# Kernel tuning notes

Measured on AMD Instinct MI355X. Metric: run time of the kernel, lower is better.

Reference implementation:

```python
import jax, jax.numpy as jnp
import numpy as np

B, N, L, S, H, E = 4, 8, 512, 512, 8, 64  # e == d (value head dim)


def setup_inputs() -> dict:
    key = jax.random.key(0)
    ks = jax.random.split(key, 6)
    shp_q = (B, N, L, H, E)
    shp_kv = (B, N, S, H, E)
    return {
        "q_re": jax.random.normal(ks[0], shp_q, dtype=jnp.float32),
        "q_im": jax.random.normal(ks[1], shp_q, dtype=jnp.float32),
        "k_re": jax.random.normal(ks[2], shp_kv, dtype=jnp.float32),
        "k_im": jax.random.normal(ks[3], shp_kv, dtype=jnp.float32),
        "v_re": jax.random.normal(ks[4], shp_kv, dtype=jnp.float32),
        "v_im": jax.random.normal(ks[5], shp_kv, dtype=jnp.float32),
    }


def reference(q_re, q_im, k_re, k_im, v_re, v_im):
    # complex_mul('bnlhe,bnshe->bnhls', q, k):
    #   real = qr.kr - qi.ki ; imag = qr.ki - qi.kr  (note: NOT standard +; faithful to source)
    s_re = (jnp.einsum('bnlhe,bnshe->bnhls', q_re, k_re)
            - jnp.einsum('bnlhe,bnshe->bnhls', q_im, k_im))
    s_im = (jnp.einsum('bnlhe,bnshe->bnhls', q_re, k_im)
            - jnp.einsum('bnlhe,bnshe->bnhls', q_im, k_re))
    # softmax over |scores| along key axis s (no 1/sqrt(e) scaling in source)
    mag = jnp.sqrt(s_re * s_re + s_im * s_im)
    attn = jax.nn.softmax(mag, axis=-1)  # [b,n,h,l,s]; dropout = identity (eval)
    # scores are real-valued after softmax; complex_mul with zero imag reduces to:
    v_out_re = jnp.einsum('bnhls,bnshd->bnlhd', attn, v_re)
    v_out_im = jnp.einsum('bnhls,bnshd->bnlhd', attn, v_im)
    # stack real/imag (torch returns complex tensor) -> [2,b,n,l,h,d]
    return jnp.stack((v_out_re, v_out_im), axis=0)
```

## Files before the change

kernel.cpp:

```cpp
#include <hip/hip_runtime.h>
#include <hip/hip_fp16.h>

typedef _Float16 half8 __attribute__((ext_vector_type(8)));
typedef _Float16 half4 __attribute__((ext_vector_type(4)));
typedef __fp16  fp16x2 __attribute__((ext_vector_type(2)));
typedef float f32x4 __attribute__((ext_vector_type(4)));

#define BB 4
#define NB 8
#define LL 512
#define SS 512
#define HH 8
#define EE 64
#define ROWSTRIDE (HH * EE)

__device__ __forceinline__ unsigned pkh(float a, float b) {
    union { fp16x2 h; unsigned u; } c;
    c.h = __builtin_amdgcn_cvt_pkrtz(a, b);
    return c.u;
}


__global__ __launch_bounds__(512, 4) void cattn_kernel(
    const float* __restrict__ qre, const float* __restrict__ qim,
    const float* __restrict__ kre, const float* __restrict__ kim,
    const float* __restrict__ vre, const float* __restrict__ vim,
    float* __restrict__ out)
{
    __shared__ __align__(16) _Float16 KtRe[2][64 * 64];
    __shared__ __align__(16) _Float16 KtIm[2][64 * 64];
    __shared__ __align__(16) _Float16 VtRe[2][64 * 64];
    __shared__ __align__(16) _Float16 VtIm[2][64 * 64];
    __shared__ __align__(16) _Float16 Pbuf[8][16 * 64];

    const int tid  = threadIdx.x;
    const int wave = tid >> 6;
    const int lane = tid & 63;
    const int lgrp = lane >> 4;
    const int l16  = lane & 15;

    const int bid  = blockIdx.x;
    const int nid  = (bid & 7) * 128 + (bid >> 3);
    const int lt   = nid & 3;
    const int head = nid >> 2;
    const int h    = head & 7;
    const int bn   = head >> 3;

    const size_t headQ = (size_t)bn * LL * ROWSTRIDE + (size_t)h * EE;
    const size_t headK = (size_t)bn * SS * ROWSTRIDE + (size_t)h * EE;

    float4 ka[2], kb[2];
    float4 vv[4];

    const int kEc0  = tid & 7;
    const int kS0   = (tid >> 3) & 63;
    const int vArr  = tid >> 8;
    const int vD0   = (tid & 15) * 4;
    const int vS0   = ((tid >> 4) & 15) * 4;

    auto stage_load = [&](int st) {
        const int tb = st * 64;
        {
            const float* p = kre + headK + (size_t)(tb + kS0) * ROWSTRIDE + kEc0 * 8;
            ka[0] = *(const float4*)p;
            kb[0] = *(const float4*)(p + 4);
        }
        {
            const float* p = kim + headK + (size_t)(tb + kS0) * ROWSTRIDE + kEc0 * 8;
            ka[1] = *(const float4*)p;
            kb[1] = *(const float4*)(p + 4);
        }
        {
            const float* src = vArr ? vim : vre;
            #pragma unroll
            for (int i = 0; i < 4; ++i)
                vv[i] = *(const float4*)(src + headK + (size_t)(tb + vS0 + i) * ROWSTRIDE + vD0);
        }
    };

    auto stage_write = [&](int buf) {
        #pragma unroll
        for (int it = 0; it < 2; ++it) {
            union { half8 h; unsigned u[4]; } kv;
            kv.u[0] = pkh(ka[it].x, ka[it].y);
            kv.u[1] = pkh(ka[it].z, ka[it].w);
            kv.u[2] = pkh(kb[it].x, kb[it].y);
            kv.u[3] = pkh(kb[it].z, kb[it].w);
            _Float16* base = it ? KtIm[buf] : KtRe[buf];
            *reinterpret_cast<half8*>(reinterpret_cast<char*>(base) +
                kS0 * 128 + ((kEc0 * 16) ^ ((kS0 & 7) << 4))) = kv.h;
        }
        {
            _Float16* base = vArr ? VtIm[buf] : VtRe[buf];
            #pragma unroll
            for (int dd = 0; dd < 4; ++dd) {
                int d = vD0 + dd;
                union { half4 h; unsigned u[2]; } hv;
                hv.u[0] = pkh((&vv[0].x)[dd], (&vv[1].x)[dd]);
                hv.u[1] = pkh((&vv[2].x)[dd], (&vv[3].x)[dd]);
                *reinterpret_cast<half4*>(reinterpret_cast<char*>(base) +
                    d * 128 + ((vS0 * 2) ^ ((d & 7) << 4))) = hv.h;
            }
        }
    };

    const int l0 = lt * 128 + wave * 16;
    half8 qr[2], qin[2];
    {
        size_t base = headQ + (size_t)(l0 + l16) * ROWSTRIDE + lgrp * 8;
        #pragma unroll
        for (int ec = 0; ec < 2; ++ec) {
            float4 a0 = *(const float4*)(qre + base + ec * 32);
            float4 a1 = *(const float4*)(qre + base + ec * 32 + 4);
            float4 b0 = *(const float4*)(qim + base + ec * 32);
            float4 b1 = *(const float4*)(qim + base + ec * 32 + 4);
            #pragma unroll
            for (int j = 0; j < 4; ++j) {
                qr[ec][j]      = (_Float16)((&a0.x)[j]);
                qr[ec][4 + j]  = (_Float16)((&a1.x)[j]);
                qin[ec][j]     = (_Float16)(-(&b0.x)[j]);
                qin[ec][4 + j] = (_Float16)(-(&b1.x)[j]);
            }
        }
    }

    f32x4 ore[4], oim[4];
    #pragma unroll
    for (int n = 0; n < 4; ++n) { ore[n] = (f32x4){0.f,0.f,0.f,0.f}; oim[n] = (f32x4){0.f,0.f,0.f,0.f}; }
    float m = -1e30f, lsum = 0.f;

    stage_load(0);
    stage_write(0);
    __syncthreads();

    char* Pw = reinterpret_cast<char*>(&Pbuf[wave][0]);
    const int prow = l16 * 128;
    const int pswz = (l16 & 7) << 4;

    for (int st = 0; st < 8; ++st) {
        const int cur = st & 1;
        if (st < 7) stage_load(st + 1);

        const char* KR = (const char*)KtRe[cur];
        const char* KI = (const char*)KtIm[cur];
        const char* VR = (const char*)VtRe[cur];
        const char* VI = (const char*)VtIm[cur];

        float p_[4][4];
        float tmax = 0.f;
        #pragma unroll
        for (int n = 0; n < 4; ++n) {
            int srow = n * 16 + l16;
            int rb   = srow * 128;
            int swz  = (srow & 7) << 4;
            half8 kr0 = *(const half8*)(KR + rb + ((lgrp * 16)      ^ swz));
            half8 kr1 = *(const half8*)(KR + rb + ((64 + lgrp * 16) ^ swz));
            half8 ki0 = *(const half8*)(KI + rb + ((lgrp * 16)      ^ swz));
            half8 ki1 = *(const half8*)(KI + rb + ((64 + lgrp * 16) ^ swz));
            f32x4 z = (f32x4){0.f,0.f,0.f,0.f};
            z = __builtin_amdgcn_mfma_f32_16x16x32_f16(kr0, qr[0],  z, 0, 0, 0);
            z = __builtin_amdgcn_mfma_f32_16x16x32_f16(kr1, qr[1],  z, 0, 0, 0);
            z = __builtin_amdgcn_mfma_f32_16x16x32_f16(ki0, qin[0], z, 0, 0, 0);
            z = __builtin_amdgcn_mfma_f32_16x16x32_f16(ki1, qin[1], z, 0, 0, 0);
            f32x4 w = (f32x4){0.f,0.f,0.f,0.f};
            w = __builtin_amdgcn_mfma_f32_16x16x32_f16(ki0, qr[0],  w, 0, 0, 0);
            w = __builtin_amdgcn_mfma_f32_16x16x32_f16(ki1, qr[1],  w, 0, 0, 0);
            w = __builtin_amdgcn_mfma_f32_16x16x32_f16(kr0, qin[0], w, 0, 0, 0);
            w = __builtin_amdgcn_mfma_f32_16x16x32_f16(kr1, qin[1], w, 0, 0, 0);
            #pragma unroll
            for (int r = 0; r < 4; ++r) {
                float mg = __builtin_amdgcn_sqrtf(z[r] * z[r] + w[r] * w[r]);
                p_[n][r] = mg;
                tmax = fmaxf(tmax, mg);
            }
        }

        tmax = fmaxf(tmax, __shfl_xor(tmax, 16));
        tmax = fmaxf(tmax, __shfl_xor(tmax, 32));
        float mn = fmaxf(m, tmax);
        if (__any(tmax > m)) {
            float sc = __expf(m - mn);
            lsum *= sc;
            float scr[4];
            #pragma unroll
            for (int r = 0; r < 4; ++r) scr[r] = __shfl(sc, lgrp * 4 + r);
            #pragma unroll
            for (int n = 0; n < 4; ++n)
                #pragma unroll
                for (int r = 0; r < 4; ++r) { ore[n][r] *= scr[r]; oim[n][r] *= scr[r]; }
        }
        m = mn;
        #pragma unroll
        for (int n = 0; n < 4; ++n)
            #pragma unroll
            for (int r = 0; r < 4; ++r) {
                float pe = __expf(p_[n][r] - mn);
                p_[n][r] = pe;
                lsum += pe;
            }

        #pragma unroll
        for (int n = 0; n < 4; ++n) {
            uint2 val;
            val.x = pkh(p_[n][0], p_[n][1]);
            val.y = pkh(p_[n][2], p_[n][3]);
            *reinterpret_cast<uint2*>(Pw + prow + ((n * 32 + lgrp * 8) ^ pswz)) = val;
        }

        #pragma unroll
        for (int kc = 0; kc < 2; ++kc) {
            half8 pa = *reinterpret_cast<const half8*>(Pw + prow + ((kc * 64 + lgrp * 16) ^ pswz));
            int sb2 = (kc * 32 + lgrp * 8) * 2;
            #pragma unroll
            for (int nd = 0; nd < 4; ++nd) {
                int d  = nd * 16 + l16;
                int vo = d * 128 + (sb2 ^ ((d & 7) << 4));
                half8 vr = *(const half8*)(VR + vo);
                half8 vi = *(const half8*)(VI + vo);
                ore[nd] = __builtin_amdgcn_mfma_f32_16x16x32_f16(pa, vr, ore[nd], 0, 0, 0);
                oim[nd] = __builtin_amdgcn_mfma_f32_16x16x32_f16(pa, vi, oim[nd], 0, 0, 0);
            }
        }

        if (st < 7) stage_write(cur ^ 1);
        __syncthreads();
    }

    lsum += __shfl_xor(lsum, 16);
    lsum += __shfl_xor(lsum, 32);
    const size_t outImOff = (size_t)BB * NB * LL * HH * EE;
    #pragma unroll
    for (int r = 0; r < 4; ++r) {
        int lrow = l0 + lgrp * 4 + r;
        float ls  = __shfl(lsum, lgrp * 4 + r);
        float inv = 1.f / ls;
        size_t obase = ((size_t)bn * LL + lrow) * ROWSTRIDE + (size_t)h * EE;
        #pragma unroll
        for (int nd = 0; nd < 4; ++nd) {
            int d = nd * 16 + l16;
            out[obase + d]            = ore[nd][r] * inv;
            out[outImOff + obase + d] = oim[nd][r] * inv;
        }
    }
}

extern "C" void kernel_launch(void* const* d_in, const int* in_sizes, int n_in,
                              void* d_out, int out_size, void* d_ws, size_t ws_size,
                              hipStream_t stream) {
    const float* qre = (const float*)d_in[0];
    const float* qim = (const float*)d_in[1];
    const float* kre = (const float*)d_in[2];
    const float* kim = (const float*)d_in[3];
    const float* vre = (const float*)d_in[4];
    const float* vim = (const float*)d_in[5];
    float* out = (float*)d_out;
    dim3 grid(1024), block(512);
    hipLaunchKernelGGL(cattn_kernel, grid, block, 0, stream,
                       qre, qim, kre, kim, vre, vim, out);
}
```

Baseline: 87.45 us.

## Software-pipeline QK scores of next tile with softmax/PV of current tile

Restructures the key-tile loop so the QK score MFMAs for tile t+1 are issued before the softmax and PV MFMAs for tile t, using two register sets of scores. This aims to overlap the exp/sqrt/shuffle work with matrix-core work and hide LDS latency. It adds an extra __syncthreads per stage and more live registers, which may cut occupancy under the 512x4 launch bound. The row-sum reduction now happens per tile.

```diff
diff --git a/kernel.cpp b/kernel.cpp
--- a/kernel.cpp
+++ b/kernel.cpp
@@ -20,6 +20,94 @@
     return c.u;
 }
 
+
+#define QK_PHASE(KRB, KIB, PP, MX) do {                                        \
+    float tmax_ = 0.f;                                                         \
+    const char* KR_ = (const char*)(KRB);                                      \
+    const char* KI_ = (const char*)(KIB);                                      \
+    _Pragma("unroll")                                                          \
+    for (int n = 0; n < 4; ++n) {                                              \
+        int srow = n * 16 + l16;                                               \
+        int rb   = srow * 128;                                                 \
+        int swz  = (srow & 7) << 4;                                            \
+        half8 kr0 = *(const half8*)(KR_ + rb + ((lgrp * 16)      ^ swz));      \
+        half8 kr1 = *(const half8*)(KR_ + rb + ((64 + lgrp * 16) ^ swz));      \
+        half8 ki0 = *(const half8*)(KI_ + rb + ((lgrp * 16)      ^ swz));      \
+        half8 ki1 = *(const half8*)(KI_ + rb + ((64 + lgrp * 16) ^ swz));      \
+        f32x4 z = (f32x4){0.f,0.f,0.f,0.f};                                    \
+        z = __builtin_amdgcn_mfma_f32_16x16x32_f16(kr0, qr[0],  z, 0, 0, 0);   \
+        z = __builtin_amdgcn_mfma_f32_16x16x32_f16(kr1, qr[1],  z, 0, 0, 0);   \
+        z = __builtin_amdgcn_mfma_f32_16x16x32_f16(ki0, qin[0], z, 0, 0, 0);   \
+        z = __builtin_amdgcn_mfma_f32_16x16x32_f16(ki1, qin[1], z, 0, 0, 0);   \
+        f32x4 w = (f32x4){0.f,0.f,0.f,0.f};                                    \
+        w = __builtin_amdgcn_mfma_f32_16x16x32_f16(ki0, qr[0],  w, 0, 0, 0);   \
+        w = __builtin_amdgcn_mfma_f32_16x16x32_f16(ki1, qr[1],  w, 0, 0, 0);   \
+        w = __builtin_amdgcn_mfma_f32_16x16x32_f16(kr0, qin[0], w, 0, 0, 0);   \
+        w = __builtin_amdgcn_mfma_f32_16x16x32_f16(kr1, qin[1], w, 0, 0, 0);   \
+        _Pragma("unroll")                                                      \
+        for (int r = 0; r < 4; ++r) {                                          \
+            float mg = __builtin_amdgcn_sqrtf(z[r] * z[r] + w[r] * w[r]);      \
+            PP[n][r] = mg;                                                     \
+            tmax_ = fmaxf(tmax_, mg);                                          \
+        }                                                                      \
+    }                                                                          \
+    MX = tmax_;                                                                \
+} while (0)
+
+#define FINISH_PHASE(VRB, VIB, PP, MX) do {                                    \
+    float tmax_ = fmaxf(MX, __shfl_xor(MX, 16));                               \
+    tmax_ = fmaxf(tmax_, __shfl_xor(tmax_, 32));                               \
+    float mn_ = fmaxf(m, tmax_);                                               \
+    if (__any(tmax_ > m)) {                                                    \
+        float sc_ = __expf(m - mn_);                                           \
+        lsum *= sc_;                                                           \
+        float scr_[4];                                                         \
+        _Pragma("unroll")                                                      \
+        for (int r = 0; r < 4; ++r) scr_[r] = __shfl(sc_, lgrp * 4 + r);       \
+        _Pragma("unroll")                                                      \
+        for (int n = 0; n < 4; ++n) {                                          \
+            _Pragma("unroll")                                                  \
+            for (int r = 0; r < 4; ++r) {                                      \
+                ore[n][r] *= scr_[r];                                          \
+                oim[n][r] *= scr_[r];                                          \
+            }                                                                  \
+        }                                                                      \
+    }                                                                          \
+    m = mn_;                                                                   \
+    float ps_ = 0.f;                                                           \
+    _Pragma("unroll")                                                          \
+    for (int n = 0; n < 4; ++n) {                                              \
+        _Pragma("unroll")                                                      \
+        for (int r = 0; r < 4; ++r) {                                          \
+            float pe_ = __expf(PP[n][r] - mn_);                                \
+            PP[n][r] = pe_;                                                    \
+            ps_ += pe_;                                                        \
+        }                                                                      \
+        uint2 val_;                                                            \
+        val_.x = pkh(PP[n][0], PP[n][1]);                                      \
+        val_.y = pkh(PP[n][2], PP[n][3]);                                      \
+        *reinterpret_cast<uint2*>(Pw + prow + ((n * 32 + lgrp * 8) ^ pswz)) = val_; \
+    }                                                                          \
+    ps_ += __shfl_xor(ps_, 16);                                                \
+    ps_ += __shfl_xor(ps_, 32);                                                \
+    lsum += ps_;                                                               \
+    const char* VR_ = (const char*)(VRB);                                      \
+    const char* VI_ = (const char*)(VIB);                                      \
+    _Pragma("unroll")                                                          \
+    for (int kc = 0; kc < 2; ++kc) {                                           \
+        half8 pa_ = *reinterpret_cast<const half8*>(Pw + prow + ((kc * 64 + lgrp * 16) ^ pswz)); \
+        int sb2_ = (kc * 32 + lgrp * 8) * 2;                                   \
+        _Pragma("unroll")                                                      \
+        for (int nd = 0; nd < 4; ++nd) {                                       \
+            int d_  = nd * 16 + l16;                                           \
+            int vo_ = d_ * 128 + (sb2_ ^ ((d_ & 7) << 4));                     \
+            half8 vr_ = *(const half8*)(VR_ + vo_);                            \
+            half8 vi_ = *(const half8*)(VI_ + vo_);                            \
+            ore[nd] = __builtin_amdgcn_mfma_f32_16x16x32_f16(pa_, vr_, ore[nd], 0, 0, 0); \
+            oim[nd] = __builtin_amdgcn_mfma_f32_16x16x32_f16(pa_, vi_, oim[nd], 0, 0, 0); \
+        }                                                                      \
+    }                                                                          \
+} while (0)
 
 __global__ __launch_bounds__(512, 4) void cattn_kernel(
     const float* __restrict__ qre, const float* __restrict__ qim,
@@ -129,105 +217,41 @@
     for (int n = 0; n < 4; ++n) { ore[n] = (f32x4){0.f,0.f,0.f,0.f}; oim[n] = (f32x4){0.f,0.f,0.f,0.f}; }
     float m = -1e30f, lsum = 0.f;
 
+    char* Pw = reinterpret_cast<char*>(&Pbuf[wave][0]);
+    const int prow = l16 * 128;
+    const int pswz = (l16 & 7) << 4;
+
+    float pA[4][4], pB[4][4];
+    float mxA, mxB;
+
     stage_load(0);
     stage_write(0);
     __syncthreads();
 
-    char* Pw = reinterpret_cast<char*>(&Pbuf[wave][0]);
-    const int prow = l16 * 128;
-    const int pswz = (l16 & 7) << 4;
-
-    for (int st = 0; st < 8; ++st) {
-        const int cur = st & 1;
-        if (st < 7) stage_load(st + 1);
-
-        const char* KR = (const char*)KtRe[cur];
-        const char* KI = (const char*)KtIm[cur];
-        const char* VR = (const char*)VtRe[cur];
-        const char* VI = (const char*)VtIm[cur];
-
-        float p_[4][4];
-        float tmax = 0.f;
-        #pragma unroll
-        for (int n = 0; n < 4; ++n) {
-            int srow = n * 16 + l16;
-            int rb   = srow * 128;
-            int swz  = (srow & 7) << 4;
-            half8 kr0 = *(const half8*)(KR + rb + ((lgrp * 16)      ^ swz));
-            half8 kr1 = *(const half8*)(KR + rb + ((64 + lgrp * 16) ^ swz));
-            half8 ki0 = *(const half8*)(KI + rb + ((lgrp * 16)      ^ swz));
-            half8 ki1 = *(const half8*)(KI + rb + ((64 + lgrp * 16) ^ swz));
-            f32x4 z = (f32x4){0.f,0.f,0.f,0.f};
-            z = __builtin_amdgcn_mfma_f32_16x16x32_f16(kr0, qr[0],  z, 0, 0, 0);
-            z = __builtin_amdgcn_mfma_f32_16x16x32_f16(kr1, qr[1],  z, 0, 0, 0);
-            z = __builtin_amdgcn_mfma_f32_16x16x32_f16(ki0, qin[0], z, 0, 0, 0);
-            z = __builtin_amdgcn_mfma_f32_16x16x32_f16(ki1, qin[1], z, 0, 0, 0);
-            f32x4 w = (f32x4){0.f,0.f,0.f,0.f};
-            w = __builtin_amdgcn_mfma_f32_16x16x32_f16(ki0, qr[0],  w, 0, 0, 0);
-            w = __builtin_amdgcn_mfma_f32_16x16x32_f16(ki1, qr[1],  w, 0, 0, 0);
-            w = __builtin_amdgcn_mfma_f32_16x16x32_f16(kr0, qin[0], w, 0, 0, 0);
-            w = __builtin_amdgcn_mfma_f32_16x16x32_f16(kr1, qin[1], w, 0, 0, 0);
-            #pragma unroll
-            for (int r = 0; r < 4; ++r) {
-                float mg = __builtin_amdgcn_sqrtf(z[r] * z[r] + w[r] * w[r]);
-                p_[n][r] = mg;
-                tmax = fmaxf(tmax, mg);
-            }
-        }
-
-        tmax = fmaxf(tmax, __shfl_xor(tmax, 16));
-        tmax = fmaxf(tmax, __shfl_xor(tmax, 32));
-        float mn = fmaxf(m, tmax);
-        if (__any(tmax > m)) {
-            float sc = __expf(m - mn);
-            lsum *= sc;
-            float scr[4];
-            #pragma unroll
-            for (int r = 0; r < 4; ++r) scr[r] = __shfl(sc, lgrp * 4 + r);
-            #pragma unroll
-            for (int n = 0; n < 4; ++n)
-                #pragma unroll
-                for (int r = 0; r < 4; ++r) { ore[n][r] *= scr[r]; oim[n][r] *= scr[r]; }
-        }
-        m = mn;
-        #pragma unroll
-        for (int n = 0; n < 4; ++n)
-            #pragma unroll
-            for (int r = 0; r < 4; ++r) {
-                float pe = __expf(p_[n][r] - mn);
-                p_[n][r] = pe;
-                lsum += pe;
-            }
-
-        #pragma unroll
-        for (int n = 0; n < 4; ++n) {
-            uint2 val;
-            val.x = pkh(p_[n][0], p_[n][1]);
-            val.y = pkh(p_[n][2], p_[n][3]);
-            *reinterpret_cast<uint2*>(Pw + prow + ((n * 32 + lgrp * 8) ^ pswz)) = val;
-        }
-
-        #pragma unroll
-        for (int kc = 0; kc < 2; ++kc) {
-            half8 pa = *reinterpret_cast<const half8*>(Pw + prow + ((kc * 64 + lgrp * 16) ^ pswz));
-            int sb2 = (kc * 32 + lgrp * 8) * 2;
-            #pragma unroll
-            for (int nd = 0; nd < 4; ++nd) {
-                int d  = nd * 16 + l16;
-                int vo = d * 128 + (sb2 ^ ((d & 7) << 4));
-                half8 vr = *(const half8*)(VR + vo);
-                half8 vi = *(const half8*)(VI + vo);
-                ore[nd] = __builtin_amdgcn_mfma_f32_16x16x32_f16(pa, vr, ore[nd], 0, 0, 0);
-                oim[nd] = __builtin_amdgcn_mfma_f32_16x16x32_f16(pa, vi, oim[nd], 0, 0, 0);
-            }
-        }
-
-        if (st < 7) stage_write(cur ^ 1);
+    stage_load(1);
+    QK_PHASE(KtRe[0], KtIm[0], pA, mxA);
+    stage_write(1);
+    __syncthreads();
+
+    for (int tp = 0; tp < 3; ++tp) {
+        stage_load(2 * tp + 2);
+        QK_PHASE(KtRe[1], KtIm[1], pB, mxB);
+        FINISH_PHASE(VtRe[0], VtIm[0], pA, mxA);
+        __syncthreads();
+        stage_write(0);
+        __syncthreads();
+        stage_load(2 * tp + 3);
+        QK_PHASE(KtRe[0], KtIm[0], pA, mxA);
+        FINISH_PHASE(VtRe[1], VtIm[1], pB, mxB);
+        __syncthreads();
+        stage_write(1);
         __syncthreads();
     }
 
-    lsum += __shfl_xor(lsum, 16);
-    lsum += __shfl_xor(lsum, 32);
+    QK_PHASE(KtRe[1], KtIm[1], pB, mxB);
+    FINISH_PHASE(VtRe[0], VtIm[0], pA, mxA);
+    FINISH_PHASE(VtRe[1], VtIm[1], pB, mxB);
+
     const size_t outImOff = (size_t)BB * NB * LL * HH * EE;
     #pragma unroll
     for (int r = 0; r < 4; ++r) {
```

New measurement: 278.0 us. +217.9%, slower.
